# Kernel optimization log

Hardware: AMD Instinct MI355X
Metric: run time of the kernel (lower is better)

## Reference

```python
import jax, jax.numpy as jnp
import numpy as np

B, N, C = 2, 2048, 768
H = 12
HD = C // H  # 64


def setup_inputs() -> dict:
    key = jax.random.key(0)
    ks = jax.random.split(key, 6)
    s = 0.02
    x = jax.random.normal(ks[0], (B, N, C), dtype=jnp.float32)
    xpos = jnp.arange(B * N, dtype=jnp.int64).reshape(B, N) % N
    W_qkv = jax.random.normal(ks[1], (3 * C, C), dtype=jnp.float32) * s
    b_qkv = jnp.zeros((3 * C,), dtype=jnp.float32)
    W_proj = jax.random.normal(ks[2], (C, C), dtype=jnp.float32) * s
    b_proj = jnp.zeros((C,), dtype=jnp.float32)
    return {"x": x, "xpos": xpos, "W_qkv": W_qkv, "b_qkv": b_qkv,
            "W_proj": W_proj, "b_proj": b_proj}


def reference(x, xpos, W_qkv, b_qkv, W_proj, b_proj):
    # rope is None in this configuration -> xpos is unused, matching torch module.
    Bx, Nx, Cx = x.shape
    scale = (Cx // H) ** -0.5
    qkv = x @ W_qkv.T + b_qkv                     # [B, N, 3C]
    qkv = qkv.reshape(Bx, Nx, 3, H, HD)
    q = jnp.einsum('bnhd->bhnd', qkv[:, :, 0])    # [B, H, N, HD]
    k = jnp.einsum('bnhd->bhnd', qkv[:, :, 1])
    v = jnp.einsum('bnhd->bhnd', qkv[:, :, 2])
    attn = jnp.einsum('bhnd,bhmd->bhnm', q, k) * scale  # [B, H, N, N]
    attn = jax.nn.softmax(attn, axis=-1)
    out = jnp.einsum('bhnm,bhmd->bhnd', attn, v)  # [B, H, N, HD]
    out = jnp.einsum('bhnd->bnhd', out).reshape(Bx, Nx, Cx)
    return out @ W_proj.T + b_proj
```

## Files before the change

### kernel.cpp

```cpp
#include <hip/hip_runtime.h>
#include <hip/hip_bf16.h>


typedef _Float16 half8 __attribute__((ext_vector_type(8)));
typedef _Float16 half4_t __attribute__((ext_vector_type(4)));
typedef float floatx4 __attribute__((ext_vector_type(4)));
typedef float floatx16 __attribute__((ext_vector_type(16)));
typedef unsigned int uintx4 __attribute__((ext_vector_type(4)));
typedef unsigned int uintx2 __attribute__((ext_vector_type(2)));

#define SCALE_LOG2E 0.1803368801111204f

constexpr int XH_OFF    = 0;
constexpr int WQKV_OFF  = XH_OFF + 4096 * 768;
constexpr int WPROJ_OFF = WQKV_OFF + 2304 * 768;
constexpr int QK_OFF    = WPROJ_OFF + 768 * 768;
constexpr int VTH_OFF   = QK_OFF + 4096 * 1536;
constexpr int PO_OFF    = VTH_OFF + 24 * 64 * 2048;
constexpr int PSTAT_OFF = PO_OFF + 2 * 24 * 2048 * 64;

__device__ __forceinline__ void gl16(const _Float16* g, _Float16* l) {
  __builtin_amdgcn_global_load_lds(
      (const __attribute__((address_space(1))) unsigned int*)g,
      (__attribute__((address_space(3))) unsigned int*)l, 16, 0, 0);
}

__global__ __launch_bounds__(256) void cvt_all(const float* __restrict__ x,
                                               const float* __restrict__ wqkv,
                                               const float* __restrict__ wproj,
                                               _Float16* __restrict__ ws) {
  constexpr int n1 = 4096 * 768 / 4;
  constexpr int n2 = 2304 * 768 / 4;
  int i = blockIdx.x * 256 + threadIdx.x;
  const float* src; _Float16* dst; int j;
  if (i < n1)           { src = x;     dst = ws + XH_OFF;    j = i; }
  else if (i < n1 + n2) { src = wqkv;  dst = ws + WQKV_OFF;  j = i - n1; }
  else                  { src = wproj; dst = ws + WPROJ_OFF; j = i - n1 - n2; }
  floatx4 f = *(const floatx4*)(src + 4 * j);
  half4_t h;
  h[0] = (_Float16)f[0]; h[1] = (_Float16)f[1];
  h[2] = (_Float16)f[2]; h[3] = (_Float16)f[3];
  *(half4_t*)(dst + 4 * j) = h;
}

__global__ __launch_bounds__(256) void qkv_gemm(const _Float16* __restrict__ xh,
                                                const _Float16* __restrict__ wh,
                                                const float* __restrict__ bias,
                                                _Float16* __restrict__ qkh,
                                                _Float16* __restrict__ vth) {
  __shared__ __align__(16) _Float16 sA[2][128 * 64];
  __shared__ __align__(16) _Float16 sB[2][128 * 64];
  const int tid = threadIdx.x;
  const int nblk = blockIdx.x % 18, mblk = blockIdx.x / 18;
  const int lane = tid & 63, w = tid >> 6;
  const int q31 = lane & 31, hi = lane >> 5;
  const int lrow = lane >> 3;
  const int lchunk = (lane & 7) ^ lrow;
  const int wq = w >> 1, wn = w & 1;

  floatx16 acc[2][2];
#pragma unroll
  for (int mr = 0; mr < 2; ++mr)
#pragma unroll
    for (int nc = 0; nc < 2; ++nc)
#pragma unroll
      for (int i = 0; i < 16; ++i) acc[mr][nc][i] = 0.f;

  auto stage = [&](int kt, int sel) {
#pragma unroll
    for (int i = 0; i < 8; ++i) {
      int g = i * 32 + w * 8;
      if (g < 128)
        gl16(xh + (mblk * 128 + g + lrow) * 768 + kt * 64 + lchunk * 8,
             &sA[sel][g * 64]);
      else
        gl16(wh + (nblk * 128 + (g - 128) + lrow) * 768 + kt * 64 + lchunk * 8,
             &sB[sel][(g - 128) * 64]);
    }
  };

  stage(0, 0);

  for (int kt = 0; kt < 12; ++kt) {
    __builtin_amdgcn_s_barrier();
    if (kt < 11) {
      stage(kt + 1, (kt + 1) & 1);
      asm volatile("s_waitcnt vmcnt(8)" ::: "memory");
    } else {
      asm volatile("s_waitcnt vmcnt(0)" ::: "memory");
    }
    const _Float16* cA = sA[kt & 1];
    const _Float16* cB = sB[kt & 1];
#pragma unroll
    for (int c = 0; c < 4; ++c) {
      half8 af[2], bf[2];
#pragma unroll
      for (int mr = 0; mr < 2; ++mr) {
        int row = wq * 64 + mr * 32 + q31;
        af[mr] = *(const half8*)(cA + row * 64 + (((c * 2 + hi) ^ (row & 7)) * 8));
      }
#pragma unroll
      for (int nc = 0; nc < 2; ++nc) {
        int row = wn * 64 + nc * 32 + q31;
        bf[nc] = *(const half8*)(cB + row * 64 + (((c * 2 + hi) ^ (row & 7)) * 8));
      }
#pragma unroll
      for (int mr = 0; mr < 2; ++mr)
#pragma unroll
        for (int nc = 0; nc < 2; ++nc)
          acc[mr][nc] = __builtin_amdgcn_mfma_f32_32x32x16_f16(af[mr], bf[nc], acc[mr][nc], 0, 0, 0);
    }
  }

#pragma unroll
  for (int mr = 0; mr < 2; ++mr) {
    const int tok0 = mblk * 128 + wq * 64 + mr * 32;
#pragma unroll
    for (int nc = 0; nc < 2; ++nc) {
      int cbase = nblk * 128 + wn * 64 + nc * 32;
      int col = cbase + q31;
      float bv = bias[col];
      if (cbase < 1536) {
        float sc = (cbase < 768) ? SCALE_LOG2E : 1.0f;
#pragma unroll
        for (int r = 0; r < 16; ++r) {
          int token = tok0 + (r & 3) + 8 * (r >> 2) + 4 * hi;
          qkh[token * 1536 + col] = (_Float16)((acc[mr][nc][r] + bv) * sc);
        }
      } else {
        int dcol = cbase - 1536 + q31;
        int h = dcol >> 6, d = dcol & 63;
        int bh = (tok0 >> 11) * 12 + h;
#pragma unroll
        for (int g2 = 0; g2 < 4; ++g2) {
          int n0 = (tok0 & 2047) + g2 * 8 + hi * 4;
          half4_t hv;
#pragma unroll
          for (int e = 0; e < 4; ++e) hv[e] = (_Float16)(acc[mr][nc][g2 * 4 + e] + bv);
          *(half4_t*)(vth + (bh * 64 + d) * 2048 + n0) = hv;
        }
      }
    }
  }
}

__global__ __launch_bounds__(256, 4) void attn_fused(const _Float16* __restrict__ qkh,
                                                     const _Float16* __restrict__ vth,
                                                     _Float16* __restrict__ pO,
                                                     float* __restrict__ pL) {
  __shared__ __align__(16) _Float16 sK[2][64 * 64];
  __shared__ __align__(16) _Float16 sVT[2][64 * 64];
  const int tid = threadIdx.x;
  const int bx = blockIdx.x;
  const int bh = bx % 24;
  const int rest = bx / 24;
  const int ks = rest & 1, qt = rest >> 1;
  const int b = bh / 12, h = bh % 12;
  const int lane = tid & 63, w = tid >> 6;
  const int q = lane & 31, hi = lane >> 5;

  const int qkbase = b * 2048 * 1536 + h * 64;
  const int qrow = qt * 128 + w * 32 + q;

  half8 qf[4];
#pragma unroll
  for (int c = 0; c < 4; ++c)
    qf[c] = *(const half8*)(qkh + qkbase + qrow * 1536 + c * 16 + hi * 8);

  const int l3 = lane >> 3;
  const int lc = (lane & 7) ^ l3;
  const int key0 = ks * 1024;
  const _Float16* kbase = qkh + qkbase + 768 + (key0 + w * 8 + l3) * 1536 + lc * 8;
  const _Float16* vbase = vth + (bh * 64 + w * 8 + l3) * 2048 + key0 + lc * 8;

  floatx16 O[2];
#pragma unroll
  for (int dg = 0; dg < 2; ++dg)
#pragma unroll
    for (int i = 0; i < 16; ++i) O[dg][i] = 0.f;
  float lrow = 0.f;

  auto stage = [&](int kt, int bufsel) {
    _Float16* dK = (_Float16*)sK[bufsel] + w * 512;
    _Float16* dV = (_Float16*)sVT[bufsel] + w * 512;
    const _Float16* kc = kbase + kt * 64 * 1536;
    const _Float16* vc = vbase + kt * 64;
    gl16(kc, dK);
    gl16(kc + 32 * 1536, dK + 2048);
    gl16(vc, dV);
    gl16(vc + 32 * 2048, dV + 2048);
  };

  stage(0, 0);

  for (int kt = 0; kt < 16; ++kt) {
    __builtin_amdgcn_s_barrier();
    if (kt < 15) {
      stage(kt + 1, (kt + 1) & 1);
      asm volatile("s_waitcnt vmcnt(4)" ::: "memory");
    } else {
      asm volatile("s_waitcnt vmcnt(0)" ::: "memory");
    }
    const _Float16* cK = &sK[kt & 1][0];
    const _Float16* cV = &sVT[kt & 1][0];

    float rsum = 0.f;
#pragma unroll
    for (int og = 0; og < 2; ++og) {
      floatx16 s;
#pragma unroll
      for (int i = 0; i < 16; ++i) s[i] = 0.f;
      const int krow = og * 32 + q;
#pragma unroll
      for (int c = 0; c < 4; ++c) {
        half8 kf = *(const half8*)(cK + krow * 64 + (((c * 2 + hi) ^ (krow & 7)) * 8));
        s = __builtin_amdgcn_mfma_f32_32x32x16_f16(kf, qf[c], s, 0, 0, 0);
      }

#pragma unroll
      for (int mm = 0; mm < 2; ++mm) {
        const int rb = mm * 8;
        float e0 = __builtin_amdgcn_exp2f(s[rb + 0]);
        float e1 = __builtin_amdgcn_exp2f(s[rb + 1]);
        float e2 = __builtin_amdgcn_exp2f(s[rb + 2]);
        float e3 = __builtin_amdgcn_exp2f(s[rb + 3]);
        float e4 = __builtin_amdgcn_exp2f(s[rb + 4]);
        float e5 = __builtin_amdgcn_exp2f(s[rb + 5]);
        float e6 = __builtin_amdgcn_exp2f(s[rb + 6]);
        float e7 = __builtin_amdgcn_exp2f(s[rb + 7]);
        rsum += ((e0 + e1) + (e2 + e3)) + ((e4 + e5) + (e6 + e7));
        unsigned ua = __builtin_bit_cast(unsigned, __builtin_amdgcn_cvt_pkrtz(e0, e1));
        unsigned ub = __builtin_bit_cast(unsigned, __builtin_amdgcn_cvt_pkrtz(e2, e3));
        unsigned uc = __builtin_bit_cast(unsigned, __builtin_amdgcn_cvt_pkrtz(e4, e5));
        unsigned ud = __builtin_bit_cast(unsigned, __builtin_amdgcn_cvt_pkrtz(e6, e7));
        uintx2 sAC = __builtin_amdgcn_permlane32_swap(ua, uc, false, false);
        uintx2 sBD = __builtin_amdgcn_permlane32_swap(ub, ud, false, false);
        uintx4 u; u[0] = sAC[0]; u[1] = sBD[0]; u[2] = sAC[1]; u[3] = sBD[1];
        half8 bfrag = __builtin_bit_cast(half8, u);

        const int rc2 = (og * 2 + mm) * 2 + hi;
#pragma unroll
        for (int dg = 0; dg < 2; ++dg) {
          const int vrow = dg * 32 + q;
          half8 vf = *(const half8*)(cV + vrow * 64 + ((rc2 ^ (vrow & 7)) * 8));
          O[dg] = __builtin_amdgcn_mfma_f32_32x32x16_f16(vf, bfrag, O[dg], 0, 0, 0);
        }
      }
    }
    lrow += rsum;
  }

  const int prow = (ks * 24 + bh) * 2048 + qt * 128 + w * 32;
#pragma unroll
  for (int dg = 0; dg < 2; ++dg)
#pragma unroll
    for (int g2 = 0; g2 < 4; ++g2) {
      half4_t hv;
#pragma unroll
      for (int e = 0; e < 4; ++e) hv[e] = (_Float16)O[dg][g2 * 4 + e];
      *(half4_t*)(pO + (prow + q) * 64 + dg * 32 + g2 * 8 + hi * 4) = hv;
    }
  lrow += __shfl_xor(lrow, 32, 64);
  if (lane < 32) pL[prow + lane] = lrow;
}

__global__ __launch_bounds__(256) void proj_gemm(const _Float16* __restrict__ pO,
                                                 const float* __restrict__ pL,
                                                 const _Float16* __restrict__ wh,
                                                 const float* __restrict__ bias,
                                                 float* __restrict__ out) {
  __shared__ __align__(16) _Float16 sA[64 * 64];
  __shared__ __align__(16) _Float16 sB[128 * 64];
  const int tid = threadIdx.x;
  const int nblk = blockIdx.x % 6, mblk = blockIdx.x / 6;
  const int lane = tid & 63, w = tid >> 6;
  const int q31 = lane & 31, hi = lane >> 5;
  const int lrow = lane >> 3;
  const int lchunk = (lane & 7) ^ lrow;
  const int wq = w >> 1, wn = w & 1;
  const int arow = tid >> 2, achk = tid & 3;
  const int tok0 = mblk * 64;
  const int b = tok0 >> 11, tokl = tok0 & 2047;

  floatx16 acc[2];
#pragma unroll
  for (int nc = 0; nc < 2; ++nc)
#pragma unroll
    for (int i = 0; i < 16; ++i) acc[nc][i] = 0.f;

  for (int kt = 0; kt < 12; ++kt) {
    const int bh = b * 12 + kt;
    const int row1 = bh * 2048 + tokl + arow;
    const int row2 = (24 + bh) * 2048 + tokl + arow;
    float f = 1.0f / (pL[row1] + pL[row2]);

    if (kt) __syncthreads();
#pragma unroll
    for (int i = 0; i < 4; ++i) {
      int g = i * 32 + w * 8;
      gl16(wh + (nblk * 128 + g + lrow) * 768 + kt * 64 + lchunk * 8, sB + g * 64);
    }
#pragma unroll
    for (int cc = 0; cc < 2; ++cc) {
      int c8 = achk + 4 * cc;
      half8 o1 = *(const half8*)(pO + row1 * 64 + c8 * 8);
      half8 o2 = *(const half8*)(pO + row2 * 64 + c8 * 8);
      half8 o;
#pragma unroll
      for (int e = 0; e < 8; ++e)
        o[e] = (_Float16)(f * ((float)o1[e] + (float)o2[e]));
      *(half8*)(sA + arow * 64 + ((c8 ^ (arow & 7)) * 8)) = o;
    }
    __syncthreads();

#pragma unroll
    for (int c = 0; c < 4; ++c) {
      const int arow2 = wq * 32 + q31;
      half8 af = *(const half8*)(sA + arow2 * 64 + (((c * 2 + hi) ^ (arow2 & 7)) * 8));
      half8 bf[2];
#pragma unroll
      for (int nc = 0; nc < 2; ++nc) {
        int row = wn * 64 + nc * 32 + q31;
        bf[nc] = *(const half8*)(sB + row * 64 + (((c * 2 + hi) ^ (row & 7)) * 8));
      }
#pragma unroll
      for (int nc = 0; nc < 2; ++nc)
        acc[nc] = __builtin_amdgcn_mfma_f32_32x32x16_f16(af, bf[nc], acc[nc], 0, 0, 0);
    }
  }

  const int mtok0 = mblk * 64 + wq * 32;
#pragma unroll
  for (int nc = 0; nc < 2; ++nc) {
    int col = nblk * 128 + wn * 64 + nc * 32 + q31;
    float bv = bias[col];
#pragma unroll
    for (int r = 0; r < 16; ++r) {
      int token = mtok0 + (r & 3) + 8 * (r >> 2) + 4 * hi;
      out[token * 768 + col] = acc[nc][r] + bv;
    }
  }
}

extern "C" void kernel_launch(void* const* d_in, const int* in_sizes, int n_in,
                              void* d_out, int out_size, void* d_ws, size_t ws_size,
                              hipStream_t stream) {
  const float* x     = (const float*)d_in[0];
  const float* wqkv  = (const float*)d_in[2];
  const float* bqkv  = (const float*)d_in[3];
  const float* wproj = (const float*)d_in[4];
  const float* bproj = (const float*)d_in[5];
  float* out = (float*)d_out;

  _Float16* ws = (_Float16*)d_ws;
  _Float16* xh     = ws + XH_OFF;
  _Float16* wqkvh  = ws + WQKV_OFF;
  _Float16* wprojh = ws + WPROJ_OFF;
  _Float16* qkh    = ws + QK_OFF;
  _Float16* vth    = ws + VTH_OFF;
  _Float16* pO     = ws + PO_OFF;
  float*    pL     = (float*)(ws + PSTAT_OFF);

  constexpr int total_v4 = (4096 * 768 + 2304 * 768 + 768 * 768) / 4;
  cvt_all<<<total_v4 / 256, 256, 0, stream>>>(x, wqkv, wproj, ws);
  qkv_gemm<<<32 * 18, 256, 0, stream>>>(xh, wqkvh, bqkv, qkh, vth);
  attn_fused<<<24 * 32, 256, 0, stream>>>(qkh, vth, pO, pL);
  proj_gemm<<<64 * 6, 256, 0, stream>>>(pO, pL, wprojh, bproj, out);
}
```

Baseline: 170.4 us.

## Drop attention key-split; normalize output in-kernel and simplify proj GEMM

The attention kernel no longer splits the keys into two halves. Each block now has 2 waves covering 64 queries and loops over all 32 key tiles. It divides by the row sum itself and writes a normalized fp16 output in token-major layout, so the projection GEMM no longer has to merge partials. The projection becomes a plain double-buffered GEMM that loads its A tile straight into LDS. The QKV GEMM and attention loops replace the hand-tuned vmcnt waits with __syncthreads. The cost is about half as many resident waves and a longer serial loop per attention block, which may weaken latency hiding.

After: 181.8 us. +6.7%, slower.

```diff
diff --git a/kernel.cpp b/kernel.cpp
--- a/kernel.cpp
+++ b/kernel.cpp
@@ -16,8 +16,7 @@
 constexpr int WPROJ_OFF = WQKV_OFF + 2304 * 768;
 constexpr int QK_OFF    = WPROJ_OFF + 768 * 768;
 constexpr int VTH_OFF   = QK_OFF + 4096 * 1536;
-constexpr int PO_OFF    = VTH_OFF + 24 * 64 * 2048;
-constexpr int PSTAT_OFF = PO_OFF + 2 * 24 * 2048 * 64;
+constexpr int OH_OFF    = VTH_OFF + 24 * 64 * 2048;
 
 __device__ __forceinline__ void gl16(const _Float16* g, _Float16* l) {
   __builtin_amdgcn_global_load_lds(
@@ -82,13 +81,8 @@
   stage(0, 0);
 
   for (int kt = 0; kt < 12; ++kt) {
-    __builtin_amdgcn_s_barrier();
-    if (kt < 11) {
-      stage(kt + 1, (kt + 1) & 1);
-      asm volatile("s_waitcnt vmcnt(8)" ::: "memory");
-    } else {
-      asm volatile("s_waitcnt vmcnt(0)" ::: "memory");
-    }
+    __syncthreads();
+    if (kt < 11) stage(kt + 1, (kt + 1) & 1);
     const _Float16* cA = sA[kt & 1];
     const _Float16* cB = sB[kt & 1];
 #pragma unroll
@@ -144,23 +138,21 @@
   }
 }
 
-__global__ __launch_bounds__(256, 4) void attn_fused(const _Float16* __restrict__ qkh,
+__global__ __launch_bounds__(128, 2) void attn_fused(const _Float16* __restrict__ qkh,
                                                      const _Float16* __restrict__ vth,
-                                                     _Float16* __restrict__ pO,
-                                                     float* __restrict__ pL) {
+                                                     _Float16* __restrict__ oh) {
   __shared__ __align__(16) _Float16 sK[2][64 * 64];
   __shared__ __align__(16) _Float16 sVT[2][64 * 64];
   const int tid = threadIdx.x;
   const int bx = blockIdx.x;
   const int bh = bx % 24;
-  const int rest = bx / 24;
-  const int ks = rest & 1, qt = rest >> 1;
+  const int qt = bx / 24;
   const int b = bh / 12, h = bh % 12;
   const int lane = tid & 63, w = tid >> 6;
   const int q = lane & 31, hi = lane >> 5;
 
   const int qkbase = b * 2048 * 1536 + h * 64;
-  const int qrow = qt * 128 + w * 32 + q;
+  const int qrow = qt * 64 + w * 32 + q;
 
   half8 qf[4];
 #pragma unroll
@@ -169,9 +161,8 @@
 
   const int l3 = lane >> 3;
   const int lc = (lane & 7) ^ l3;
-  const int key0 = ks * 1024;
-  const _Float16* kbase = qkh + qkbase + 768 + (key0 + w * 8 + l3) * 1536 + lc * 8;
-  const _Float16* vbase = vth + (bh * 64 + w * 8 + l3) * 2048 + key0 + lc * 8;
+  const _Float16* kbase = qkh + qkbase + 768 + (w * 8 + l3) * 1536 + lc * 8;
+  const _Float16* vbase = vth + (bh * 64 + w * 8 + l3) * 2048 + lc * 8;
 
   floatx16 O[2];
 #pragma unroll
@@ -185,22 +176,18 @@
     _Float16* dV = (_Float16*)sVT[bufsel] + w * 512;
     const _Float16* kc = kbase + kt * 64 * 1536;
     const _Float16* vc = vbase + kt * 64;
-    gl16(kc, dK);
-    gl16(kc + 32 * 1536, dK + 2048);
-    gl16(vc, dV);
-    gl16(vc + 32 * 2048, dV + 2048);
+#pragma unroll
+    for (int k2 = 0; k2 < 4; ++k2) {
+      gl16(kc + k2 * 16 * 1536, dK + k2 * 1024);
+      gl16(vc + k2 * 16 * 2048, dV + k2 * 1024);
+    }
   };
 
   stage(0, 0);
 
-  for (int kt = 0; kt < 16; ++kt) {
-    __builtin_amdgcn_s_barrier();
-    if (kt < 15) {
-      stage(kt + 1, (kt + 1) & 1);
-      asm volatile("s_waitcnt vmcnt(4)" ::: "memory");
-    } else {
-      asm volatile("s_waitcnt vmcnt(0)" ::: "memory");
-    }
+  for (int kt = 0; kt < 32; ++kt) {
+    __syncthreads();
+    if (kt < 31) stage(kt + 1, (kt + 1) & 1);
     const _Float16* cK = &sK[kt & 1][0];
     const _Float16* cV = &sVT[kt & 1][0];
 
@@ -250,27 +237,26 @@
     lrow += rsum;
   }
 
-  const int prow = (ks * 24 + bh) * 2048 + qt * 128 + w * 32;
+  lrow += __shfl_xor(lrow, 32, 64);
+  const float inv = 1.0f / lrow;
+  const int token = b * 2048 + qt * 64 + w * 32 + q;
 #pragma unroll
   for (int dg = 0; dg < 2; ++dg)
 #pragma unroll
     for (int g2 = 0; g2 < 4; ++g2) {
       half4_t hv;
 #pragma unroll
-      for (int e = 0; e < 4; ++e) hv[e] = (_Float16)O[dg][g2 * 4 + e];
-      *(half4_t*)(pO + (prow + q) * 64 + dg * 32 + g2 * 8 + hi * 4) = hv;
-    }
-  lrow += __shfl_xor(lrow, 32, 64);
-  if (lane < 32) pL[prow + lane] = lrow;
-}
-
-__global__ __launch_bounds__(256) void proj_gemm(const _Float16* __restrict__ pO,
-                                                 const float* __restrict__ pL,
+      for (int e = 0; e < 4; ++e) hv[e] = (_Float16)(O[dg][g2 * 4 + e] * inv);
+      *(half4_t*)(oh + token * 768 + h * 64 + dg * 32 + g2 * 8 + hi * 4) = hv;
+    }
+}
+
+__global__ __launch_bounds__(256) void proj_gemm(const _Float16* __restrict__ oh,
                                                  const _Float16* __restrict__ wh,
                                                  const float* __restrict__ bias,
                                                  float* __restrict__ out) {
-  __shared__ __align__(16) _Float16 sA[64 * 64];
-  __shared__ __align__(16) _Float16 sB[128 * 64];
+  __shared__ __align__(16) _Float16 sA[2][64 * 64];
+  __shared__ __align__(16) _Float16 sB[2][128 * 64];
   const int tid = threadIdx.x;
   const int nblk = blockIdx.x % 6, mblk = blockIdx.x / 6;
   const int lane = tid & 63, w = tid >> 6;
@@ -278,9 +264,6 @@
   const int lrow = lane >> 3;
   const int lchunk = (lane & 7) ^ lrow;
   const int wq = w >> 1, wn = w & 1;
-  const int arow = tid >> 2, achk = tid & 3;
-  const int tok0 = mblk * 64;
-  const int b = tok0 >> 11, tokl = tok0 & 2047;
 
   floatx16 acc[2];
 #pragma unroll
@@ -288,40 +271,35 @@
 #pragma unroll
     for (int i = 0; i < 16; ++i) acc[nc][i] = 0.f;
 
-  for (int kt = 0; kt < 12; ++kt) {
-    const int bh = b * 12 + kt;
-    const int row1 = bh * 2048 + tokl + arow;
-    const int row2 = (24 + bh) * 2048 + tokl + arow;
-    float f = 1.0f / (pL[row1] + pL[row2]);
-
-    if (kt) __syncthreads();
+  auto stage = [&](int kt, int sel) {
+    gl16(oh + (mblk * 64 + w * 8 + lrow) * 768 + kt * 64 + lchunk * 8,
+         &sA[sel][(w * 8) * 64]);
+    gl16(oh + (mblk * 64 + 32 + w * 8 + lrow) * 768 + kt * 64 + lchunk * 8,
+         &sA[sel][(32 + w * 8) * 64]);
 #pragma unroll
     for (int i = 0; i < 4; ++i) {
       int g = i * 32 + w * 8;
-      gl16(wh + (nblk * 128 + g + lrow) * 768 + kt * 64 + lchunk * 8, sB + g * 64);
-    }
-#pragma unroll
-    for (int cc = 0; cc < 2; ++cc) {
-      int c8 = achk + 4 * cc;
-      half8 o1 = *(const half8*)(pO + row1 * 64 + c8 * 8);
-      half8 o2 = *(const half8*)(pO + row2 * 64 + c8 * 8);
-      half8 o;
-#pragma unroll
-      for (int e = 0; e < 8; ++e)
-        o[e] = (_Float16)(f * ((float)o1[e] + (float)o2[e]));
-      *(half8*)(sA + arow * 64 + ((c8 ^ (arow & 7)) * 8)) = o;
-    }
+      gl16(wh + (nblk * 128 + g + lrow) * 768 + kt * 64 + lchunk * 8,
+           &sB[sel][g * 64]);
+    }
+  };
+
+  stage(0, 0);
+
+  for (int kt = 0; kt < 12; ++kt) {
     __syncthreads();
-
+    if (kt < 11) stage(kt + 1, (kt + 1) & 1);
+    const _Float16* cA = sA[kt & 1];
+    const _Float16* cB = sB[kt & 1];
 #pragma unroll
     for (int c = 0; c < 4; ++c) {
       const int arow2 = wq * 32 + q31;
-      half8 af = *(const half8*)(sA + arow2 * 64 + (((c * 2 + hi) ^ (arow2 & 7)) * 8));
+      half8 af = *(const half8*)(cA + arow2 * 64 + (((c * 2 + hi) ^ (arow2 & 7)) * 8));
       half8 bf[2];
 #pragma unroll
       for (int nc = 0; nc < 2; ++nc) {
         int row = wn * 64 + nc * 32 + q31;
-        bf[nc] = *(const half8*)(sB + row * 64 + (((c * 2 + hi) ^ (row & 7)) * 8));
+        bf[nc] = *(const half8*)(cB + row * 64 + (((c * 2 + hi) ^ (row & 7)) * 8));
       }
 #pragma unroll
       for (int nc = 0; nc < 2; ++nc)
@@ -358,12 +336,11 @@
   _Float16* wprojh = ws + WPROJ_OFF;
   _Float16* qkh    = ws + QK_OFF;
   _Float16* vth    = ws + VTH_OFF;
-  _Float16* pO     = ws + PO_OFF;
-  float*    pL     = (float*)(ws + PSTAT_OFF);
+  _Float16* oh     = ws + OH_OFF;
 
   constexpr int total_v4 = (4096 * 768 + 2304 * 768 + 768 * 768) / 4;
   cvt_all<<<total_v4 / 256, 256, 0, stream>>>(x, wqkv, wproj, ws);
   qkv_gemm<<<32 * 18, 256, 0, stream>>>(xh, wqkvh, bqkv, qkh, vth);
-  attn_fused<<<24 * 32, 256, 0, stream>>>(qkh, vth, pO, pL);
-  proj_gemm<<<64 * 6, 256, 0, stream>>>(pO, pL, wprojh, bproj, out);
-}
+  attn_fused<<<24 * 32, 128, 0, stream>>>(qkh, vth, oh);
+  proj_gemm<<<64 * 6, 256, 0, stream>>>(oh, wprojh, bproj, out);
+}
```
